# Kernel optimization log

Measured on AMD Instinct MI355X. Metric: run time of the kernel, lower is better.

## Reference

```python
import jax, jax.numpy as jnp
import numpy as np

N = 20000
NEG_SLOPE = 0.2


def gat_conv(x, src, dst, W, att_src, att_dst, bias, heads, ch, concat):
    # x: [N, F_in]; src/dst: [E] (messages flow src -> dst, softmax grouped by dst)
    n = x.shape[0]
    h = (x @ W).reshape(n, heads, ch)                      # [N, H, C]
    a_s = jnp.sum(h * att_src, axis=-1)                    # [N, H]
    a_d = jnp.sum(h * att_dst, axis=-1)                    # [N, H]
    e = jax.nn.leaky_relu(a_s[src] + a_d[dst], NEG_SLOPE)  # [E, H]
    m = jax.ops.segment_max(e, dst, num_segments=n)        # segment-softmax (stable)
    ex = jnp.exp(e - m[dst])
    denom = jax.ops.segment_sum(ex, dst, num_segments=n)
    alpha = ex / (denom[dst] + 1e-16)                      # [E, H]
    msg = h[src] * alpha[:, :, None]                       # [E, H, C]
    out = jax.ops.segment_sum(msg, dst, num_segments=n)    # [N, H, C]
    out = out.reshape(n, heads * ch) if concat else out.mean(axis=1)
    return out + bias


def setup_inputs() -> dict:
    key = jax.random.key(0)
    ks = jax.random.split(key, 24)
    in_ch, h_ch, out_ch, H, OH = 512, 128, 64, 4, 6
    hid = H * h_ch  # 512
    s = 0.1
    d = {
        "x": jax.random.normal(ks[0], (N, in_ch), jnp.float32),
        "edge_index": jax.random.randint(ks[1], (2, 160000), 0, N, jnp.int32),
        "W1": jax.random.normal(ks[2], (in_ch, H * h_ch), jnp.float32) * s,
        "as1": jax.random.normal(ks[3], (1, H, h_ch), jnp.float32) * s,
        "ad1": jax.random.normal(ks[4], (1, H, h_ch), jnp.float32) * s,
        "b1": jnp.zeros((H * h_ch,), jnp.float32),
        "lW1": jax.random.normal(ks[5], (in_ch, hid), jnp.float32) * s,
        "lb1": jnp.zeros((hid,), jnp.float32),
        "W2": jax.random.normal(ks[6], (hid, H * h_ch), jnp.float32) * s,
        "as2": jax.random.normal(ks[7], (1, H, h_ch), jnp.float32) * s,
        "ad2": jax.random.normal(ks[8], (1, H, h_ch), jnp.float32) * s,
        "b2": jnp.zeros((H * h_ch,), jnp.float32),
        "lW2": jax.random.normal(ks[9], (hid, hid), jnp.float32) * s,
        "lb2": jnp.zeros((hid,), jnp.float32),
        "W3": jax.random.normal(ks[10], (hid, OH * out_ch), jnp.float32) * s,
        "as3": jax.random.normal(ks[11], (1, OH, out_ch), jnp.float32) * s,
        "ad3": jax.random.normal(ks[12], (1, OH, out_ch), jnp.float32) * s,
        "b3": jnp.zeros((out_ch,), jnp.float32),
        "lW3": jax.random.normal(ks[13], (hid, out_ch), jnp.float32) * s,
        "lb3": jnp.zeros((out_ch,), jnp.float32),
    }
    return d


def reference(x, edge_index, W1, as1, ad1, b1, lW1, lb1,
              W2, as2, ad2, b2, lW2, lb2,
              W3, as3, ad3, b3, lW3, lb3):
    n = x.shape[0]
    loops = jnp.arange(n, dtype=edge_index.dtype)  # PyG GATConv add_self_loops=True
    src = jnp.concatenate([edge_index[0], loops])
    dst = jnp.concatenate([edge_index[1], loops])
    h = jax.nn.elu(gat_conv(x, src, dst, W1, as1, ad1, b1, 4, 128, True) + x @ lW1 + lb1)
    h = jax.nn.elu(gat_conv(h, src, dst, W2, as2, ad2, b2, 4, 128, True) + h @ lW2 + lb2)
    out = gat_conv(h, src, dst, W3, as3, ad3, b3, 6, 64, False) + h @ lW3 + lb3
    return out
```

## Files before the change

kernel.cpp:

```cpp
#include <hip/hip_runtime.h>
#include <cstddef>
#include <cstdint>
#include <type_traits>

#define N_NODES 20000
#define NPAD 20096
#define E0_EDGES 160000
#define E_TOT (E0_EDGES + N_NODES)
#define CAP 64

typedef __bf16 bf16x8 __attribute__((ext_vector_type(8)));
typedef float f32x4 __attribute__((ext_vector_type(4)));

__device__ __forceinline__ ushort f2bf(float f) {
  uint32_t u = __float_as_uint(f);
  return (ushort)((u + 0x7FFFu + ((u >> 16) & 1u)) >> 16);
}
__device__ __forceinline__ float bf2f(ushort h) {
  return __uint_as_float((uint32_t)h << 16);
}

__device__ __forceinline__ int SW(int r) { return ((r >> 1) & 3) ^ ((r >> 3) & 1); }

#define GLOAD16(g, l)                                                         \
  __builtin_amdgcn_global_load_lds(                                           \
      (const __attribute__((address_space(1))) void*)(uintptr_t)(g),          \
      (__attribute__((address_space(3))) void*)(uint32_t)(uintptr_t)(l),      \
      16, 0, 0)


__global__ void fill_csr_kernel(const int* __restrict__ ei, int* __restrict__ cnt,
                                int* __restrict__ slots) {
  int e = blockIdx.x * blockDim.x + threadIdx.x;
  if (e >= E_TOT) return;
  int src, dst;
  if (e < E0_EDGES) { src = ei[e]; dst = ei[E0_EDGES + e]; }
  else              { src = e - E0_EDGES; dst = src; }
  int pos = atomicAdd(&cnt[dst], 1);
  if (pos < CAP) slots[dst * CAP + pos] = src;
}


__global__ void convert_x_kernel(const float* __restrict__ x, ushort* __restrict__ xb) {
  size_t i = ((size_t)blockIdx.x * blockDim.x + threadIdx.x) * 4;
  if (i >= (size_t)NPAD * 512) return;
  if (i < (size_t)N_NODES * 512) {
    float4 v = *(const float4*)(x + i);
    ushort4 o;
    o.x = f2bf(v.x); o.y = f2bf(v.y); o.z = f2bf(v.z); o.w = f2bf(v.w);
    *(ushort4*)(xb + i) = o;
  } else {
    *(ushort4*)(xb + i) = make_ushort4(0, 0, 0, 0);
  }
}

__global__ void transpose_all_kernel(
    const float* __restrict__ W1, const float* __restrict__ lW1,
    const float* __restrict__ W2, const float* __restrict__ lW2,
    const float* __restrict__ W3, const float* __restrict__ lW3,
    ushort* __restrict__ Bt1, ushort* __restrict__ Bt2, ushort* __restrict__ Bt3) {
  __shared__ float tile[32][33];
  const int K = 512;
  int z = blockIdx.z;
  const float* W; ushort* B; int M;
  switch (z) {
    case 0:  W = W1;  B = Bt1;              M = 512; break;
    case 1:  W = lW1; B = Bt1 + 512 * 512;  M = 512; break;
    case 2:  W = W2;  B = Bt2;              M = 512; break;
    case 3:  W = lW2; B = Bt2 + 512 * 512;  M = 512; break;
    case 4:  W = W3;  B = Bt3;              M = 384; break;
    default: W = lW3; B = Bt3 + 384 * 512;  M = 64;  break;
  }
  int mb = blockIdx.x * 32, kb = blockIdx.y * 32;
  if (mb >= M) return;
  int tx = threadIdx.x, ty = threadIdx.y;
#pragma unroll
  for (int i = 0; i < 32; i += 8)
    tile[ty + i][tx] = W[(size_t)(kb + ty + i) * M + mb + tx];
  __syncthreads();
#pragma unroll
  for (int i = 0; i < 32; i += 8)
    B[(size_t)(mb + ty + i) * K + kb + tx] = f2bf(tile[tx][ty + i]);
}


template <typename Out1T>
__global__ __launch_bounds__(256, 4) void mfma_gemm_kernel(
    const ushort* __restrict__ A,
    const ushort* __restrict__ Bt,
    ushort* __restrict__ out0, int ld0, int split,
    Out1T* __restrict__ out1, int ld1, int Mout1, const float* __restrict__ bias1,
    const float* __restrict__ att_sw, const float* __restrict__ att_dw,
    float* __restrict__ a_sp, float* __restrict__ a_dp,
    int nheads, int headC,
    int K, int NT, int nwg) {
  __shared__ __attribute__((aligned(16))) ushort As[3][128][32];
  __shared__ __attribute__((aligned(16))) ushort Bs[3][128][32];

  int q = nwg >> 3, r = nwg & 7;
  int orig = blockIdx.x;
  int xcd = orig & 7, pos = orig >> 3;
  int wgid = (xcd < r ? xcd * (q + 1) : r * (q + 1) + (xcd - r) * q) + pos;
  int by = wgid / NT, bx = wgid - by * NT;
  int bm = by * 128, bn = bx * 128;

  int tid = threadIdx.x, lane = tid & 63, wave = tid >> 6;
  int wrow = (wave >> 1) * 64, wcol = (wave & 1) * 64;

  size_t K2 = (size_t)K * 2;
  int rofs = lane >> 2;
  int gch = (lane & 3) ^ SW(rofs);
  const char* pA[2];
  const char* pB[2];
  int srow[2];
#pragma unroll
  for (int it = 0; it < 2; ++it) {
    int rr = wave * 32 + it * 16 + rofs;
    srow[it] = wave * 32 + it * 16;
    pA[it] = (const char*)A + (size_t)(bm + rr) * K2 + gch * 16;
    pB[it] = (const char*)Bt + (size_t)(bn + rr) * K2 + gch * 16;
  }

  int fr = lane & 15, hi = lane >> 4;
  int rch = hi ^ SW(fr);

  f32x4 acc[4][4] = {};

  char* AsB = (char*)&As[0][0][0];
  char* BsB = (char*)&Bs[0][0][0];

#pragma unroll
  for (int s = 0; s < 2; ++s) {
#pragma unroll
    for (int it = 0; it < 2; ++it) {
      GLOAD16(pA[it], AsB + s * 8192 + srow[it] * 64);
      GLOAD16(pB[it], BsB + s * 8192 + srow[it] * 64);
    }
#pragma unroll
    for (int it = 0; it < 2; ++it) { pA[it] += 64; pB[it] += 64; }
  }

  const int KSTEPS = K >> 5;
  int s_cur = 0, s_stage = 2;
  for (int k = 0; k < KSTEPS; ++k) {
    if (k + 1 < KSTEPS) {
      asm volatile("s_waitcnt vmcnt(4)" ::: "memory");
    } else {
      asm volatile("s_waitcnt vmcnt(0)" ::: "memory");
    }
    __builtin_amdgcn_s_barrier();
    asm volatile("" ::: "memory");
    if (k + 2 < KSTEPS) {
#pragma unroll
      for (int it = 0; it < 2; ++it) {
        GLOAD16(pA[it], AsB + s_stage * 8192 + srow[it] * 64);
        GLOAD16(pB[it], BsB + s_stage * 8192 + srow[it] * 64);
      }
#pragma unroll
      for (int it = 0; it < 2; ++it) { pA[it] += 64; pB[it] += 64; }
    }
    {
      bf16x8 af[4], bfr[4];
#pragma unroll
      for (int i = 0; i < 4; ++i)
        af[i] = *(const bf16x8*)&As[s_cur][wrow + i * 16 + fr][rch * 8];
#pragma unroll
      for (int j = 0; j < 4; ++j)
        bfr[j] = *(const bf16x8*)&Bs[s_cur][wcol + j * 16 + fr][rch * 8];
#pragma unroll
      for (int i = 0; i < 4; ++i)
#pragma unroll
        for (int j = 0; j < 4; ++j)
          acc[i][j] = __builtin_amdgcn_mfma_f32_16x16x32_bf16(af[i], bfr[j], acc[i][j], 0, 0, 0);
    }
    asm volatile("" ::: "memory");
    s_cur = (s_cur == 2) ? 0 : s_cur + 1;
    s_stage = (s_stage == 2) ? 0 : s_stage + 1;
  }

  int colg = bn + wcol;
  bool lower = colg < split;
  int g4 = hi << 2;
  int ccol = fr;
#pragma unroll
  for (int i = 0; i < 4; ++i) {
#pragma unroll
    for (int rr = 0; rr < 4; ++rr) {
      int row = bm + wrow + g4 + i * 16 + rr;
      if (row >= N_NODES) continue;
#pragma unroll
      for (int j = 0; j < 4; ++j) {
        int col = colg + j * 16 + ccol;
        float v = acc[i][j][rr];
        if (lower) {
          out0[(size_t)row * ld0 + col] = f2bf(v);
        } else {
          int c1 = col - split;
          if (c1 < Mout1) {
            float b = v + bias1[c1];
            if constexpr (std::is_same<Out1T, ushort>::value)
              out1[(size_t)row * ld1 + c1] = f2bf(b);
            else
              out1[(size_t)row * ld1 + c1] = b;
          }
        }
      }
    }
  }

  if (lower) {
    int hd = colg / headC;
    int cb = colg - hd * headC;
    int half = (cb >> 6) & 1;
    float ws4[4], wd4[4];
#pragma unroll
    for (int j = 0; j < 4; ++j) {
      int cc = hd * headC + cb + j * 16 + ccol;
      ws4[j] = att_sw[cc];
      wd4[j] = att_dw[cc];
    }
#pragma unroll
    for (int i = 0; i < 4; ++i) {
#pragma unroll
      for (int rr = 0; rr < 4; ++rr) {
        float ps = 0.f, pd = 0.f;
#pragma unroll
        for (int j = 0; j < 4; ++j) { ps += acc[i][j][rr] * ws4[j]; pd += acc[i][j][rr] * wd4[j]; }
#pragma unroll
        for (int o = 1; o < 16; o <<= 1) { ps += __shfl_xor(ps, o); pd += __shfl_xor(pd, o); }
        if ((lane & 15) == 0) {
          int row = bm + wrow + g4 + i * 16 + rr;
          if (row < N_NODES) {
            size_t idx = ((size_t)row * nheads + hd) * 2;
            if (headC == 128) {
              a_sp[idx + half] = ps;
              a_dp[idx + half] = pd;
            } else {
              a_sp[idx] = ps;  a_sp[idx + 1] = 0.f;
              a_dp[idx] = pd;  a_dp[idx + 1] = 0.f;
            }
          }
        }
      }
    }
  }
}


template <int H, int C>
__global__ __launch_bounds__(128) void gather12_fused(
    const int* __restrict__ cnt, const int* __restrict__ slots,
    const float* __restrict__ a_sp, const float* __restrict__ a_dp,
    const ushort* __restrict__ hbuf, const float* __restrict__ gat_bias,
    const ushort* __restrict__ skip_in, ushort* __restrict__ outbuf) {
  __shared__ float al[H][CAP];
  __shared__ int srcs[CAP];
  int n = blockIdx.x;
  int t = threadIdx.x, lane = t & 63, w = t >> 6;
  int deg = min(cnt[n], CAP);

  int sj = 0;
  if (lane < deg) sj = slots[n * CAP + lane];
#pragma unroll
  for (int hh = 0; hh < 2; ++hh) {
    int hd = 2 * w + hh;
    float e = -1e30f;
    if (lane < deg) {
      size_t is = ((size_t)sj * H + hd) * 2;
      size_t id = ((size_t)n * H + hd) * 2;
      float v = a_sp[is] + a_sp[is + 1] + a_dp[id] + a_dp[id + 1];
      e = v > 0.f ? v : 0.2f * v;
    }
    float m = e;
#pragma unroll
    for (int o = 32; o > 0; o >>= 1) m = fmaxf(m, __shfl_xor(m, o));
    float ex = (lane < deg) ? expf(e - m) : 0.f;
    float s = ex;
#pragma unroll
    for (int o = 32; o > 0; o >>= 1) s += __shfl_xor(s, o);
    float inv = 1.f / (s + 1e-16f);
    if (lane < deg) al[hd][lane] = ex * inv;
  }
  if (w == 0 && lane < deg) srcs[lane] = sj;
  __syncthreads();

  int f0 = 4 * t, hd = t >> 5;
  float a0 = 0.f, a1 = 0.f, a2 = 0.f, a3 = 0.f;
  for (int j = 0; j < deg; ++j) {
    float a = al[hd][j];
    ushort4 hv = *(const ushort4*)(hbuf + (size_t)srcs[j] * (H * C) + f0);
    a0 += a * bf2f(hv.x);
    a1 += a * bf2f(hv.y);
    a2 += a * bf2f(hv.z);
    a3 += a * bf2f(hv.w);
  }
  ushort4 sk = *(const ushort4*)(skip_in + (size_t)n * (H * C) + f0);
  float o0 = a0 + gat_bias[f0 + 0] + bf2f(sk.x);
  float o1 = a1 + gat_bias[f0 + 1] + bf2f(sk.y);
  float o2 = a2 + gat_bias[f0 + 2] + bf2f(sk.z);
  float o3 = a3 + gat_bias[f0 + 3] + bf2f(sk.w);
  o0 = o0 > 0.f ? o0 : (expf(o0) - 1.f);
  o1 = o1 > 0.f ? o1 : (expf(o1) - 1.f);
  o2 = o2 > 0.f ? o2 : (expf(o2) - 1.f);
  o3 = o3 > 0.f ? o3 : (expf(o3) - 1.f);
  ushort4 ov;
  ov.x = f2bf(o0); ov.y = f2bf(o1); ov.z = f2bf(o2); ov.w = f2bf(o3);
  *(ushort4*)(outbuf + (size_t)n * (H * C) + f0) = ov;
}


__global__ __launch_bounds__(128) void gather3_fused(
    const int* __restrict__ cnt, const int* __restrict__ slots,
    const float* __restrict__ a_sp, const float* __restrict__ a_dp,
    const ushort* __restrict__ hbuf , const float* __restrict__ b3,
    float* __restrict__ out ) {
  __shared__ float al[6][CAP];
  __shared__ int srcs[CAP];
  __shared__ float part[2][64];
  int n = blockIdx.x;
  int t = threadIdx.x, lane = t & 63, w = t >> 6;
  int deg = min(cnt[n], CAP);

  int sj = 0;
  if (lane < deg) sj = slots[n * CAP + lane];
#pragma unroll
  for (int hh = 0; hh < 3; ++hh) {
    int hd = 3 * w + hh;
    float e = -1e30f;
    if (lane < deg) {
      size_t is = ((size_t)sj * 6 + hd) * 2;
      size_t id = ((size_t)n * 6 + hd) * 2;
      float v = a_sp[is] + a_sp[is + 1] + a_dp[id] + a_dp[id + 1];
      e = v > 0.f ? v : 0.2f * v;
    }
    float m = e;
#pragma unroll
    for (int o = 32; o > 0; o >>= 1) m = fmaxf(m, __shfl_xor(m, o));
    float ex = (lane < deg) ? expf(e - m) : 0.f;
    float s = ex;
#pragma unroll
    for (int o = 32; o > 0; o >>= 1) s += __shfl_xor(s, o);
    float inv = (1.f / 6.f) / (s + 1e-16f);
    if (lane < deg) al[hd][lane] = ex * inv;
  }
  if (w == 0 && lane < deg) srcs[lane] = sj;
  __syncthreads();

  int c = t & 63;
  float acc = 0.f;
  for (int j = w; j < deg; j += 2) {
    const ushort* hr = hbuf + (size_t)srcs[j] * 384 + c;
#pragma unroll
    for (int hd = 0; hd < 6; ++hd) acc += al[hd][j] * bf2f(hr[hd * 64]);
  }
  part[w][c] = acc;
  __syncthreads();
  if (t < 64) {
    size_t oi = (size_t)n * 64 + t;
    out[oi] += part[0][t] + part[1][t] + b3[t];
  }
}


extern "C" void kernel_launch(void* const* d_in, const int* in_sizes, int n_in,
                              void* d_out, int out_size, void* d_ws, size_t ws_size,
                              hipStream_t stream) {
  const float* x   = (const float*)d_in[0];
  const int*   ei  = (const int*)d_in[1];
  const float* W1  = (const float*)d_in[2];
  const float* as1 = (const float*)d_in[3];
  const float* ad1 = (const float*)d_in[4];
  const float* b1  = (const float*)d_in[5];
  const float* lW1 = (const float*)d_in[6];
  const float* lb1 = (const float*)d_in[7];
  const float* W2  = (const float*)d_in[8];
  const float* as2 = (const float*)d_in[9];
  const float* ad2 = (const float*)d_in[10];
  const float* b2  = (const float*)d_in[11];
  const float* lW2 = (const float*)d_in[12];
  const float* lb2 = (const float*)d_in[13];
  const float* W3  = (const float*)d_in[14];
  const float* as3 = (const float*)d_in[15];
  const float* ad3 = (const float*)d_in[16];
  const float* b3  = (const float*)d_in[17];
  const float* lW3 = (const float*)d_in[18];
  const float* lb3 = (const float*)d_in[19];
  float* out = (float*)d_out;

  char* ws = (char*)d_ws;
  auto alloc = [&](size_t bytes) -> void* {
    void* p = (void*)ws;
    ws += (bytes + 255) & ~(size_t)255;
    return p;
  };
  ushort* xb    = (ushort*)alloc((size_t)NPAD * 512 * 2);
  ushort* Pb    = (ushort*)alloc((size_t)NPAD * 512 * 2);
  ushort* Qb    = (ushort*)alloc((size_t)NPAD * 512 * 2);
  ushort* skipb = (ushort*)alloc((size_t)N_NODES * 512 * 2);
  ushort* hb    = (ushort*)alloc((size_t)N_NODES * 512 * 2);
  ushort* Bt1   = (ushort*)alloc((size_t)1024 * 512 * 2);
  ushort* Bt2   = (ushort*)alloc((size_t)1024 * 512 * 2);
  ushort* Bt3   = (ushort*)alloc((size_t)512 * 512 * 2);
  float*  a_sp  = (float*)alloc((size_t)N_NODES * 6 * 2 * 4);
  float*  a_dp  = (float*)alloc((size_t)N_NODES * 6 * 2 * 4);
  int*    cnt   = (int*)alloc((size_t)N_NODES * 4);
  int*    slots = (int*)alloc((size_t)N_NODES * CAP * 4);

  hipMemsetAsync(cnt, 0, N_NODES * sizeof(int), stream);
  fill_csr_kernel<<<(E_TOT + 255) / 256, 256, 0, stream>>>(ei, cnt, slots);

  convert_x_kernel<<<((NPAD * 512 / 4) + 255) / 256, 256, 0, stream>>>(x, xb);
  hipMemsetAsync(Pb + (size_t)N_NODES * 512, 0, (size_t)(NPAD - N_NODES) * 512 * 2, stream);
  hipMemsetAsync(Qb + (size_t)N_NODES * 512, 0, (size_t)(NPAD - N_NODES) * 512 * 2, stream);
  transpose_all_kernel<<<dim3(16, 16, 6), dim3(32, 8), 0, stream>>>(
      W1, lW1, W2, lW2, W3, lW3, Bt1, Bt2, Bt3);

  const int NWG12 = (NPAD / 128) * 8;
  const int NWG3  = (NPAD / 128) * 4;

  mfma_gemm_kernel<ushort><<<NWG12, 256, 0, stream>>>(
      xb, Bt1, hb, 512, 512, skipb, 512, 512, lb1, as1, ad1, a_sp, a_dp, 4, 128,
      512, 8, NWG12);
  gather12_fused<4, 128><<<N_NODES, 128, 0, stream>>>(cnt, slots, a_sp, a_dp, hb, b1, skipb, Pb);

  mfma_gemm_kernel<ushort><<<NWG12, 256, 0, stream>>>(
      Pb, Bt2, hb, 512, 512, skipb, 512, 512, lb2, as2, ad2, a_sp, a_dp, 4, 128,
      512, 8, NWG12);
  gather12_fused<4, 128><<<N_NODES, 128, 0, stream>>>(cnt, slots, a_sp, a_dp, hb, b2, skipb, Qb);

  mfma_gemm_kernel<float><<<NWG3, 256, 0, stream>>>(
      Qb, Bt3, hb, 384, 384, out, 64, 64, lb3, as3, ad3, a_sp, a_dp, 6, 64,
      512, 4, NWG3);
  gather3_fused<<<N_NODES, 128, 0, stream>>>(cnt, slots, a_sp, a_dp, hb, b3, out);
}
```

Measured before the change: 265.5 us.

## Replace LDS-staged pipelined GEMM with direct global-to-register MFMA operand loads

Removes the triple-buffered LDS staging (global_load_lds, swizzle, barriers) from the MFMA GEMM. Each wave now loads its A and B fragments straight from global memory into registers over a fully unrolled K loop. The workgroup mapping also changes to column-major (bx outer, by inner), so workgroups on the same XCD share B tiles and walk over A rows, which may help cache reuse. The cost is that operands are no longer shared between the waves of a workgroup through LDS, so global and L2 traffic rises and there is no explicit prefetch. It also drops the occupancy hint from launch_bounds and hardcodes K=512.

```diff
diff --git a/kernel.cpp b/kernel.cpp
--- a/kernel.cpp
+++ b/kernel.cpp
@@ -19,14 +19,6 @@
 __device__ __forceinline__ float bf2f(ushort h) {
   return __uint_as_float((uint32_t)h << 16);
 }
-
-__device__ __forceinline__ int SW(int r) { return ((r >> 1) & 3) ^ ((r >> 3) & 1); }
-
-#define GLOAD16(g, l)                                                         \
-  __builtin_amdgcn_global_load_lds(                                           \
-      (const __attribute__((address_space(1))) void*)(uintptr_t)(g),          \
-      (__attribute__((address_space(3))) void*)(uint32_t)(uintptr_t)(l),      \
-      16, 0, 0)
 
 
 __global__ void fill_csr_kernel(const int* __restrict__ ei, int* __restrict__ cnt,
@@ -85,7 +77,7 @@
 
 
 template <typename Out1T>
-__global__ __launch_bounds__(256, 4) void mfma_gemm_kernel(
+__global__ __launch_bounds__(256) void mfma_gemm_kernel(
     const ushort* __restrict__ A,
     const ushort* __restrict__ Bt,
     ushort* __restrict__ out0, int ld0, int split,
@@ -93,89 +85,43 @@
     const float* __restrict__ att_sw, const float* __restrict__ att_dw,
     float* __restrict__ a_sp, float* __restrict__ a_dp,
     int nheads, int headC,
-    int K, int NT, int nwg) {
-  __shared__ __attribute__((aligned(16))) ushort As[3][128][32];
-  __shared__ __attribute__((aligned(16))) ushort Bs[3][128][32];
+    int nBy, int nwg) {
+  const int K = 512;
 
   int q = nwg >> 3, r = nwg & 7;
   int orig = blockIdx.x;
   int xcd = orig & 7, pos = orig >> 3;
   int wgid = (xcd < r ? xcd * (q + 1) : r * (q + 1) + (xcd - r) * q) + pos;
-  int by = wgid / NT, bx = wgid - by * NT;
+  int bx = wgid / nBy, by = wgid - bx * nBy;
   int bm = by * 128, bn = bx * 128;
 
   int tid = threadIdx.x, lane = tid & 63, wave = tid >> 6;
   int wrow = (wave >> 1) * 64, wcol = (wave & 1) * 64;
-
-  size_t K2 = (size_t)K * 2;
-  int rofs = lane >> 2;
-  int gch = (lane & 3) ^ SW(rofs);
-  const char* pA[2];
-  const char* pB[2];
-  int srow[2];
-#pragma unroll
-  for (int it = 0; it < 2; ++it) {
-    int rr = wave * 32 + it * 16 + rofs;
-    srow[it] = wave * 32 + it * 16;
-    pA[it] = (const char*)A + (size_t)(bm + rr) * K2 + gch * 16;
-    pB[it] = (const char*)Bt + (size_t)(bn + rr) * K2 + gch * 16;
-  }
-
   int fr = lane & 15, hi = lane >> 4;
-  int rch = hi ^ SW(fr);
+
+  const char* pa[4];
+  const char* pb[4];
+#pragma unroll
+  for (int i = 0; i < 4; ++i)
+    pa[i] = (const char*)(A + (size_t)(bm + wrow + i * 16 + fr) * K + hi * 8);
+#pragma unroll
+  for (int j = 0; j < 4; ++j)
+    pb[j] = (const char*)(Bt + (size_t)(bn + wcol + j * 16 + fr) * K + hi * 8);
 
   f32x4 acc[4][4] = {};
 
-  char* AsB = (char*)&As[0][0][0];
-  char* BsB = (char*)&Bs[0][0][0];
-
-#pragma unroll
-  for (int s = 0; s < 2; ++s) {
-#pragma unroll
-    for (int it = 0; it < 2; ++it) {
-      GLOAD16(pA[it], AsB + s * 8192 + srow[it] * 64);
-      GLOAD16(pB[it], BsB + s * 8192 + srow[it] * 64);
-    }
-#pragma unroll
-    for (int it = 0; it < 2; ++it) { pA[it] += 64; pB[it] += 64; }
-  }
-
-  const int KSTEPS = K >> 5;
-  int s_cur = 0, s_stage = 2;
-  for (int k = 0; k < KSTEPS; ++k) {
-    if (k + 1 < KSTEPS) {
-      asm volatile("s_waitcnt vmcnt(4)" ::: "memory");
-    } else {
-      asm volatile("s_waitcnt vmcnt(0)" ::: "memory");
-    }
-    __builtin_amdgcn_s_barrier();
-    asm volatile("" ::: "memory");
-    if (k + 2 < KSTEPS) {
-#pragma unroll
-      for (int it = 0; it < 2; ++it) {
-        GLOAD16(pA[it], AsB + s_stage * 8192 + srow[it] * 64);
-        GLOAD16(pB[it], BsB + s_stage * 8192 + srow[it] * 64);
-      }
-#pragma unroll
-      for (int it = 0; it < 2; ++it) { pA[it] += 64; pB[it] += 64; }
-    }
-    {
-      bf16x8 af[4], bfr[4];
-#pragma unroll
-      for (int i = 0; i < 4; ++i)
-        af[i] = *(const bf16x8*)&As[s_cur][wrow + i * 16 + fr][rch * 8];
+#pragma unroll
+  for (int k = 0; k < 16; ++k) {
+    bf16x8 af[4], bf[4];
+#pragma unroll
+    for (int i = 0; i < 4; ++i) af[i] = *(const bf16x8*)(pa[i] + k * 64);
+#pragma unroll
+    for (int j = 0; j < 4; ++j) bf[j] = *(const bf16x8*)(pb[j] + k * 64);
+#pragma unroll
+    for (int i = 0; i < 4; ++i)
 #pragma unroll
       for (int j = 0; j < 4; ++j)
-        bfr[j] = *(const bf16x8*)&Bs[s_cur][wcol + j * 16 + fr][rch * 8];
-#pragma unroll
-      for (int i = 0; i < 4; ++i)
-#pragma unroll
-        for (int j = 0; j < 4; ++j)
-          acc[i][j] = __builtin_amdgcn_mfma_f32_16x16x32_bf16(af[i], bfr[j], acc[i][j], 0, 0, 0);
-    }
-    asm volatile("" ::: "memory");
-    s_cur = (s_cur == 2) ? 0 : s_cur + 1;
-    s_stage = (s_stage == 2) ? 0 : s_stage + 1;
+        acc[i][j] = __builtin_amdgcn_mfma_f32_16x16x32_bf16(af[i], bf[j], acc[i][j], 0, 0, 0);
   }
 
   int colg = bn + wcol;
@@ -415,21 +361,22 @@
   transpose_all_kernel<<<dim3(16, 16, 6), dim3(32, 8), 0, stream>>>(
       W1, lW1, W2, lW2, W3, lW3, Bt1, Bt2, Bt3);
 
-  const int NWG12 = (NPAD / 128) * 8;
-  const int NWG3  = (NPAD / 128) * 4;
+  const int NBY = NPAD / 128;
+  const int NWG12 = NBY * 8;
+  const int NWG3  = NBY * 4;
 
   mfma_gemm_kernel<ushort><<<NWG12, 256, 0, stream>>>(
       xb, Bt1, hb, 512, 512, skipb, 512, 512, lb1, as1, ad1, a_sp, a_dp, 4, 128,
-      512, 8, NWG12);
+      NBY, NWG12);
   gather12_fused<4, 128><<<N_NODES, 128, 0, stream>>>(cnt, slots, a_sp, a_dp, hb, b1, skipb, Pb);
 
   mfma_gemm_kernel<ushort><<<NWG12, 256, 0, stream>>>(
       Pb, Bt2, hb, 512, 512, skipb, 512, 512, lb2, as2, ad2, a_sp, a_dp, 4, 128,
-      512, 8, NWG12);
+      NBY, NWG12);
   gather12_fused<4, 128><<<N_NODES, 128, 0, stream>>>(cnt, slots, a_sp, a_dp, hb, b2, skipb, Qb);
 
   mfma_gemm_kernel<float><<<NWG3, 256, 0, stream>>>(
       Qb, Bt3, hb, 384, 384, out, 64, 64, lb3, as3, ad3, a_sp, a_dp, 6, 64,
-      512, 4, NWG3);
+      NBY, NWG3);
   gather3_fused<<<N_NODES, 128, 0, stream>>>(cnt, slots, a_sp, a_dp, hb, b3, out);
 }
```

Result: slower. 388.3 us (+46.3%).

## Widen GEMM tile to 128x256 with per-wave 64x128 subtiles

Applied to the files above, without the earlier changes.

Doubles the N dimension of the MFMA GEMM workgroup tile from 128 to 256 so each wave computes a 64x128 block, which doubles A-tile reuse and halves the number of workgroups. LDS for B doubles and accumulators grow to 4x8 fragments, so occupancy drops (launch bounds move from 4 to 2 waves/EU). The attention-dot epilogue is rewritten to cover a whole 128-wide head, or two 64-wide heads, per wave. K is hardcoded to 512. Fewer workgroups (about 628 for layers 1-2 and 314 for layer 3) may underfill the GPU.

```diff
diff --git a/kernel.cpp b/kernel.cpp
--- a/kernel.cpp
+++ b/kernel.cpp
@@ -85,7 +85,7 @@
 
 
 template <typename Out1T>
-__global__ __launch_bounds__(256, 4) void mfma_gemm_kernel(
+__global__ __launch_bounds__(256, 2) void mfma_gemm_kernel(
     const ushort* __restrict__ A,
     const ushort* __restrict__ Bt,
     ushort* __restrict__ out0, int ld0, int split,
@@ -93,38 +93,42 @@
     const float* __restrict__ att_sw, const float* __restrict__ att_dw,
     float* __restrict__ a_sp, float* __restrict__ a_dp,
     int nheads, int headC,
-    int K, int NT, int nwg) {
+    int NT, int nwg) {
+  const int K = 512;
   __shared__ __attribute__((aligned(16))) ushort As[3][128][32];
-  __shared__ __attribute__((aligned(16))) ushort Bs[3][128][32];
+  __shared__ __attribute__((aligned(16))) ushort Bs[3][256][32];
 
   int q = nwg >> 3, r = nwg & 7;
   int orig = blockIdx.x;
   int xcd = orig & 7, pos = orig >> 3;
   int wgid = (xcd < r ? xcd * (q + 1) : r * (q + 1) + (xcd - r) * q) + pos;
   int by = wgid / NT, bx = wgid - by * NT;
-  int bm = by * 128, bn = bx * 128;
+  int bm = by * 128, bn = bx * 256;
 
   int tid = threadIdx.x, lane = tid & 63, wave = tid >> 6;
-  int wrow = (wave >> 1) * 64, wcol = (wave & 1) * 64;
+  int wrow = (wave >> 1) * 64, wcol = (wave & 1) * 128;
 
   size_t K2 = (size_t)K * 2;
   int rofs = lane >> 2;
   int gch = (lane & 3) ^ SW(rofs);
   const char* pA[2];
-  const char* pB[2];
-  int srow[2];
+  const char* pB[4];
+  int arow[2], brow[4];
 #pragma unroll
   for (int it = 0; it < 2; ++it) {
-    int rr = wave * 32 + it * 16 + rofs;
-    srow[it] = wave * 32 + it * 16;
-    pA[it] = (const char*)A + (size_t)(bm + rr) * K2 + gch * 16;
-    pB[it] = (const char*)Bt + (size_t)(bn + rr) * K2 + gch * 16;
+    arow[it] = wave * 32 + it * 16;
+    pA[it] = (const char*)A + (size_t)(bm + arow[it] + rofs) * K2 + gch * 16;
+  }
+#pragma unroll
+  for (int it = 0; it < 4; ++it) {
+    brow[it] = wave * 64 + it * 16;
+    pB[it] = (const char*)Bt + (size_t)(bn + brow[it] + rofs) * K2 + gch * 16;
   }
 
   int fr = lane & 15, hi = lane >> 4;
   int rch = hi ^ SW(fr);
 
-  f32x4 acc[4][4] = {};
+  f32x4 acc[4][8] = {};
 
   char* AsB = (char*)&As[0][0][0];
   char* BsB = (char*)&Bs[0][0][0];
@@ -132,19 +136,20 @@
 #pragma unroll
   for (int s = 0; s < 2; ++s) {
 #pragma unroll
-    for (int it = 0; it < 2; ++it) {
-      GLOAD16(pA[it], AsB + s * 8192 + srow[it] * 64);
-      GLOAD16(pB[it], BsB + s * 8192 + srow[it] * 64);
-    }
-#pragma unroll
-    for (int it = 0; it < 2; ++it) { pA[it] += 64; pB[it] += 64; }
+    for (int it = 0; it < 2; ++it) GLOAD16(pA[it], AsB + s * 8192 + arow[it] * 64);
+#pragma unroll
+    for (int it = 0; it < 4; ++it) GLOAD16(pB[it], BsB + s * 16384 + brow[it] * 64);
+#pragma unroll
+    for (int it = 0; it < 2; ++it) pA[it] += 64;
+#pragma unroll
+    for (int it = 0; it < 4; ++it) pB[it] += 64;
   }
 
   const int KSTEPS = K >> 5;
   int s_cur = 0, s_stage = 2;
   for (int k = 0; k < KSTEPS; ++k) {
     if (k + 1 < KSTEPS) {
-      asm volatile("s_waitcnt vmcnt(4)" ::: "memory");
+      asm volatile("s_waitcnt vmcnt(6)" ::: "memory");
     } else {
       asm volatile("s_waitcnt vmcnt(0)" ::: "memory");
     }
@@ -152,26 +157,27 @@
     asm volatile("" ::: "memory");
     if (k + 2 < KSTEPS) {
 #pragma unroll
-      for (int it = 0; it < 2; ++it) {
-        GLOAD16(pA[it], AsB + s_stage * 8192 + srow[it] * 64);
-        GLOAD16(pB[it], BsB + s_stage * 8192 + srow[it] * 64);
-      }
-#pragma unroll
-      for (int it = 0; it < 2; ++it) { pA[it] += 64; pB[it] += 64; }
+      for (int it = 0; it < 2; ++it) GLOAD16(pA[it], AsB + s_stage * 8192 + arow[it] * 64);
+#pragma unroll
+      for (int it = 0; it < 4; ++it) GLOAD16(pB[it], BsB + s_stage * 16384 + brow[it] * 64);
+#pragma unroll
+      for (int it = 0; it < 2; ++it) pA[it] += 64;
+#pragma unroll
+      for (int it = 0; it < 4; ++it) pB[it] += 64;
     }
     {
-      bf16x8 af[4], bfr[4];
+      bf16x8 af[4], bf[8];
 #pragma unroll
       for (int i = 0; i < 4; ++i)
         af[i] = *(const bf16x8*)&As[s_cur][wrow + i * 16 + fr][rch * 8];
 #pragma unroll
-      for (int j = 0; j < 4; ++j)
-        bfr[j] = *(const bf16x8*)&Bs[s_cur][wcol + j * 16 + fr][rch * 8];
+      for (int j = 0; j < 8; ++j)
+        bf[j] = *(const bf16x8*)&Bs[s_cur][wcol + j * 16 + fr][rch * 8];
 #pragma unroll
       for (int i = 0; i < 4; ++i)
 #pragma unroll
-        for (int j = 0; j < 4; ++j)
-          acc[i][j] = __builtin_amdgcn_mfma_f32_16x16x32_bf16(af[i], bfr[j], acc[i][j], 0, 0, 0);
+        for (int j = 0; j < 8; ++j)
+          acc[i][j] = __builtin_amdgcn_mfma_f32_16x16x32_bf16(af[i], bf[j], acc[i][j], 0, 0, 0);
     }
     asm volatile("" ::: "memory");
     s_cur = (s_cur == 2) ? 0 : s_cur + 1;
@@ -189,7 +195,7 @@
       int row = bm + wrow + g4 + i * 16 + rr;
       if (row >= N_NODES) continue;
 #pragma unroll
-      for (int j = 0; j < 4; ++j) {
+      for (int j = 0; j < 8; ++j) {
         int col = colg + j * 16 + ccol;
         float v = acc[i][j][rr];
         if (lower) {
@@ -209,35 +215,61 @@
   }
 
   if (lower) {
-    int hd = colg / headC;
-    int cb = colg - hd * headC;
-    int half = (cb >> 6) & 1;
-    float ws4[4], wd4[4];
-#pragma unroll
-    for (int j = 0; j < 4; ++j) {
-      int cc = hd * headC + cb + j * 16 + ccol;
-      ws4[j] = att_sw[cc];
-      wd4[j] = att_dw[cc];
+    float ws8[8], wd8[8];
+    int hd0;
+    if (headC == 128) {
+      hd0 = colg >> 7;
+#pragma unroll
+      for (int j = 0; j < 8; ++j) {
+        int cc = hd0 * 128 + j * 16 + ccol;
+        ws8[j] = att_sw[cc]; wd8[j] = att_dw[cc];
+      }
+    } else {
+      hd0 = colg >> 6;
+#pragma unroll
+      for (int j = 0; j < 8; ++j) {
+        int cc = (hd0 + (j >> 2)) * 64 + (j & 3) * 16 + ccol;
+        ws8[j] = att_sw[cc]; wd8[j] = att_dw[cc];
+      }
     }
 #pragma unroll
     for (int i = 0; i < 4; ++i) {
 #pragma unroll
       for (int rr = 0; rr < 4; ++rr) {
-        float ps = 0.f, pd = 0.f;
-#pragma unroll
-        for (int j = 0; j < 4; ++j) { ps += acc[i][j][rr] * ws4[j]; pd += acc[i][j][rr] * wd4[j]; }
-#pragma unroll
-        for (int o = 1; o < 16; o <<= 1) { ps += __shfl_xor(ps, o); pd += __shfl_xor(pd, o); }
-        if ((lane & 15) == 0) {
-          int row = bm + wrow + g4 + i * 16 + rr;
-          if (row < N_NODES) {
-            size_t idx = ((size_t)row * nheads + hd) * 2;
-            if (headC == 128) {
-              a_sp[idx + half] = ps;
-              a_dp[idx + half] = pd;
-            } else {
-              a_sp[idx] = ps;  a_sp[idx + 1] = 0.f;
-              a_dp[idx] = pd;  a_dp[idx + 1] = 0.f;
+        if (headC == 128) {
+          float ps = 0.f, pd = 0.f;
+#pragma unroll
+          for (int j = 0; j < 8; ++j) { ps += acc[i][j][rr] * ws8[j]; pd += acc[i][j][rr] * wd8[j]; }
+#pragma unroll
+          for (int o = 1; o < 16; o <<= 1) { ps += __shfl_xor(ps, o); pd += __shfl_xor(pd, o); }
+          if ((lane & 15) == 0) {
+            int row = bm + wrow + g4 + i * 16 + rr;
+            if (row < N_NODES) {
+              size_t idx = ((size_t)row * nheads + hd0) * 2;
+              a_sp[idx] = ps; a_sp[idx + 1] = 0.f;
+              a_dp[idx] = pd; a_dp[idx + 1] = 0.f;
+            }
+          }
+        } else {
+          float ps0 = 0.f, pd0 = 0.f, ps1 = 0.f, pd1 = 0.f;
+#pragma unroll
+          for (int j = 0; j < 4; ++j) { ps0 += acc[i][j][rr] * ws8[j]; pd0 += acc[i][j][rr] * wd8[j]; }
+#pragma unroll
+          for (int j = 4; j < 8; ++j) { ps1 += acc[i][j][rr] * ws8[j]; pd1 += acc[i][j][rr] * wd8[j]; }
+#pragma unroll
+          for (int o = 1; o < 16; o <<= 1) {
+            ps0 += __shfl_xor(ps0, o); pd0 += __shfl_xor(pd0, o);
+            ps1 += __shfl_xor(ps1, o); pd1 += __shfl_xor(pd1, o);
+          }
+          if ((lane & 15) == 0) {
+            int row = bm + wrow + g4 + i * 16 + rr;
+            if (row < N_NODES) {
+              size_t i0 = ((size_t)row * nheads + hd0) * 2;
+              size_t i1 = ((size_t)row * nheads + hd0 + 1) * 2;
+              a_sp[i0] = ps0; a_sp[i0 + 1] = 0.f;
+              a_dp[i0] = pd0; a_dp[i0 + 1] = 0.f;
+              a_sp[i1] = ps1; a_sp[i1 + 1] = 0.f;
+              a_dp[i1] = pd1; a_dp[i1 + 1] = 0.f;
             }
           }
         }
@@ -415,21 +447,22 @@
   transpose_all_kernel<<<dim3(16, 16, 6), dim3(32, 8), 0, stream>>>(
       W1, lW1, W2, lW2, W3, lW3, Bt1, Bt2, Bt3);
 
-  const int NWG12 = (NPAD / 128) * 8;
-  const int NWG3  = (NPAD / 128) * 4;
+  const int NBY = NPAD / 128;
+  const int NWG12 = NBY * 4;
+  const int NWG3  = NBY * 2;
 
   mfma_gemm_kernel<ushort><<<NWG12, 256, 0, stream>>>(
       xb, Bt1, hb, 512, 512, skipb, 512, 512, lb1, as1, ad1, a_sp, a_dp, 4, 128,
-      512, 8, NWG12);
+      4, NWG12);
   gather12_fused<4, 128><<<N_NODES, 128, 0, stream>>>(cnt, slots, a_sp, a_dp, hb, b1, skipb, Pb);
 
   mfma_gemm_kernel<ushort><<<NWG12, 256, 0, stream>>>(
       Pb, Bt2, hb, 512, 512, skipb, 512, 512, lb2, as2, ad2, a_sp, a_dp, 4, 128,
-      512, 8, NWG12);
+      4, NWG12);
   gather12_fused<4, 128><<<N_NODES, 128, 0, stream>>>(cnt, slots, a_sp, a_dp, hb, b2, skipb, Qb);
 
   mfma_gemm_kernel<float><<<NWG3, 256, 0, stream>>>(
       Qb, Bt3, hb, 384, 384, out, 64, 64, lb3, as3, ad3, a_sp, a_dp, 6, 64,
-      512, 4, NWG3);
+      2, NWG3);
   gather3_fused<<<N_NODES, 128, 0, stream>>>(cnt, slots, a_sp, a_dp, hb, b3, out);
 }
```

Measured after the change: 305.9 us. 15.2% more time.
